# Optimization experiments

Hardware: AMD Instinct MI355X
Metric: run time of the kernel (lower is better)

Reference implementation:

```python
import jax, jax.numpy as jnp
import numpy as np

# Static configuration (from init_kwargs)
B, T, SP = 4, 100, 20          # batch, max_time_patches, max_space_patches
S = T * SP                      # flattened seq len = 2000
H, NH = 512, 8                  # hidden size, heads
D = H // NH                     # head dim = 64
CF, CB = 4, 4                   # context_forward, context_backward
ROPE_BASE = 10000.0
NEG = -1e9


def setup_inputs() -> dict:
    key = jax.random.key(0)
    ks = jax.random.split(key, 8)
    w = 1.0 / np.sqrt(H)
    x = jax.random.normal(ks[0], (B, S, H), jnp.float32)
    # token order is space-major: timestamps = time-patch id repeated per space patch
    timestamps = jnp.broadcast_to(jnp.tile(jnp.arange(T, dtype=jnp.int32), SP), (B, S))
    attn_mask = jnp.ones((B, S), jnp.int32)
    Wq = jax.random.normal(ks[1], (H, H), jnp.float32) * w
    Wk = jax.random.normal(ks[2], (H, H), jnp.float32) * w
    Wv = jax.random.normal(ks[3], (H, H), jnp.float32) * w
    Wo = jax.random.normal(ks[4], (H, H), jnp.float32) * w
    z = jnp.zeros((H,), jnp.float32)
    return {"x": x, "attn_mask": attn_mask, "timestamps": timestamps,
            "Wq": Wq, "bq": z, "Wk": Wk, "bk": z, "Wv": Wv, "bv": z,
            "Wo": Wo, "bo": z}


def _rotate_half(u):
    return jnp.concatenate((-u[..., D // 2:], u[..., :D // 2]), axis=-1)


def _rope_tables():
    inv_freq = 1.0 / (ROPE_BASE ** (jnp.arange(0, D, 2, dtype=jnp.float32) / D))
    t = jnp.arange(T, dtype=jnp.float32)
    freqs = t[:, None] * inv_freq[None, :]          # [T, D/2]
    emb = jnp.concatenate((freqs, freqs), axis=-1)  # [T, D]
    return jnp.cos(emb), jnp.sin(emb)


def _context_mask():
    # forward/backward banded window in time, tiled over space patches
    ones = jnp.ones((T, T), jnp.float32)
    m = jnp.triu(ones, k=-CF).T          # allow up to CF future time patches
    if CB > 0:
        m = m * jnp.triu(ones, k=-CB)    # allow up to CB past time patches
    return jnp.tile(m, (SP, SP))         # [S, S]


def reference(x, attn_mask, timestamps, Wq, bq, Wk, bk, Wv, bv, Wo, bo):
    # projections -> [B, NH, S, D]
    def heads(w, b):
        return (x @ w + b).reshape(B, S, NH, D).transpose(0, 2, 1, 3)
    q, k, v = heads(Wq, bq), heads(Wk, bk), heads(Wv, bv)

    # rotary position embedding indexed by time-patch timestamps
    cos_t, sin_t = _rope_tables()
    cos = cos_t[timestamps][:, None]     # [B, 1, S, D]
    sin = sin_t[timestamps][:, None]
    q = q * cos + _rotate_half(q) * sin
    k = k * cos + _rotate_half(k) * sin

    # banded-context masked attention
    scores = jnp.einsum('bhqd,bhkd->bhqk', q, k) / jnp.sqrt(jnp.float32(D))
    mask = (_context_mask()[None, None, :, :] *
            attn_mask[:, None, None, :].astype(jnp.float32)) > 0
    scores = jnp.where(mask, scores, NEG)
    attn = jax.nn.softmax(scores, axis=-1)
    out = jnp.einsum('bhqk,bhkd->bhqd', attn, v)
    out = out.transpose(0, 2, 1, 3).reshape(B, S, H)
    return out @ Wo + bo
```

## Files before the change

kernel.cpp:

```cpp
#include <hip/hip_runtime.h>
#include <hip/hip_bf16.h>
#include <stdint.h>


typedef __bf16 bf16x8 __attribute__((ext_vector_type(8)));
typedef float f32x4 __attribute__((ext_vector_type(4)));

static const size_t O_XB = 0;
static const size_t O_WT = 8192000;
static const size_t O_Q  = 10289152;
static const size_t O_K  = 18481152;
static const size_t O_V  = 26673152;
static const size_t O_RC = 34865152;
static const size_t O_RS = 34877952;
static const size_t O_VT = 34890752;

__device__ inline void gload16(const void* g, void* l) {
  __builtin_amdgcn_global_load_lds((const __attribute__((address_space(1))) void*)g,
                                   (__attribute__((address_space(3))) void*)l, 16, 0, 0);
}

__global__ __launch_bounds__(256) void prep_kernel(
    const float* __restrict__ x, const float* __restrict__ Wq, const float* __restrict__ Wk,
    const float* __restrict__ Wv, const float* __restrict__ Wo,
    __bf16* __restrict__ xb, __bf16* __restrict__ wt,
    float* __restrict__ ropeC, float* __restrict__ ropeS)
{
  const int tid = blockIdx.x * 256 + threadIdx.x;
  if (tid < 1024000) {
    float4 v = ((const float4*)x)[tid];
    union { ushort4 u; __bf16 b[4]; } p;
    p.b[0] = (__bf16)v.x; p.b[1] = (__bf16)v.y; p.b[2] = (__bf16)v.z; p.b[3] = (__bf16)v.w;
    ((ushort4*)xb)[tid] = p.u;
  }
  {
    const int mat = tid >> 18;
    const int r = tid & 262143;
    const int n = r >> 9, k = r & 511;
    const float* W = (mat == 0) ? Wq : (mat == 1) ? Wk : (mat == 2) ? Wv : Wo;
    wt[(size_t)mat * 262144 + n * 512 + k] = (__bf16)W[k * 512 + n];
  }
  if (tid < 3200) {
    const int t = tid >> 5, i = tid & 31;
    const float f = (float)t * powf(10000.0f, -(float)i / 32.0f);
    ropeC[tid] = cosf(f);
    ropeS[tid] = sinf(f);
  }
}

__device__ inline void gemm_core(const __bf16* __restrict__ A, const __bf16* __restrict__ Bm,
                                 __bf16* As, __bf16* Bs, f32x4 (&acc)[4][4],
                                 int m0, int n0, int tid, int wm, int wn, int lr, int g)
{
  const int r0 = tid >> 2;
  const int aq = tid & 3;
  for (int kk = 0; kk < 512; kk += 32) {
    int gm0 = m0 + r0;      if (gm0 > 7999) gm0 = 7999;
    int gm1 = m0 + r0 + 64; if (gm1 > 7999) gm1 = 7999;
    gload16(A + (size_t)gm0 * 512 + kk + aq * 8, As + tid * 8);
    gload16(A + (size_t)gm1 * 512 + kk + aq * 8, As + tid * 8 + 2048);
    gload16(Bm + (size_t)(n0 + r0) * 512 + kk + aq * 8, Bs + tid * 8);
    gload16(Bm + (size_t)(n0 + r0 + 64) * 512 + kk + aq * 8, Bs + tid * 8 + 2048);
    asm volatile("s_waitcnt vmcnt(0)" ::: "memory");
    __syncthreads();
    bf16x8 af[4], bfr[4];
#pragma unroll
    for (int f = 0; f < 4; ++f) {
      af[f]  = *(const bf16x8*)(As + (wm + f * 16 + lr) * 32 + g * 8);
      bfr[f] = *(const bf16x8*)(Bs + (wn + f * 16 + lr) * 32 + g * 8);
    }
#pragma unroll
    for (int i = 0; i < 4; ++i) {
#pragma unroll
      for (int j = 0; j < 4; ++j)
        acc[i][j] = __builtin_amdgcn_mfma_f32_16x16x32_bf16(af[i], bfr[j], acc[i][j], 0, 0, 0);
    }
    __syncthreads();
  }
}

__global__ __launch_bounds__(256) void qkv_gemm(
    const __bf16* __restrict__ xb, const __bf16* __restrict__ wt,
    const float* __restrict__ bq, const float* __restrict__ bk, const float* __restrict__ bv,
    const float* __restrict__ ropeC, const float* __restrict__ ropeS,
    __bf16* __restrict__ qws, __bf16* __restrict__ kws, __bf16* __restrict__ vws)
{
  const int tid = threadIdx.x;
  const int m0 = blockIdx.x * 128, n0 = blockIdx.y * 128;
  const int mat = blockIdx.z;
  __shared__ __bf16 As[4096], Bs[4096];
  f32x4 acc[4][4] = {};
  const int wid = tid >> 6, lane = tid & 63;
  const int wm = (wid >> 1) << 6, wn = (wid & 1) << 6;
  const int lr = lane & 15, g = lane >> 4;

  gemm_core(xb, wt + (size_t)mat * 262144, As, Bs, acc, m0, n0, tid, wm, wn, lr, g);

  const int hn = (n0 + wn) >> 6;
  const float* bias = (mat == 0) ? bq : (mat == 1) ? bk : bv;
  __bf16* outp = (mat == 0) ? qws : (mat == 1) ? kws : vws;
  const float qscale = (mat == 0) ? 0.125f : 1.0f;

#pragma unroll
  for (int i = 0; i < 4; ++i) {
#pragma unroll
    for (int r = 0; r < 4; ++r) {
      const int m = m0 + wm + i * 16 + g * 4 + r;
      if (m >= 8000) continue;
      const int b = m / 2000;
      const int s = m - b * 2000;
      const int t = s % 100;
      const int sp = s / 100;
      const int pos = t * 20 + sp;
      const size_t ob = ((size_t)(b * 8 + hn) * 2000 + pos) * 64;
      if (mat == 2) {
#pragma unroll
        for (int j = 0; j < 4; ++j) {
          float v = acc[i][j][r] + bias[n0 + wn + j * 16 + lr];
          outp[ob + j * 16 + lr] = (__bf16)v;
        }
      } else {
#pragma unroll
        for (int j = 0; j < 2; ++j) {
          const int dlo = j * 16 + lr;
          const float alo = acc[i][j][r]     + bias[n0 + wn + j * 16 + lr];
          const float ahi = acc[i][j + 2][r] + bias[n0 + wn + (j + 2) * 16 + lr];
          const float cs = ropeC[t * 32 + dlo], sn = ropeS[t * 32 + dlo];
          const float olo = (alo * cs - ahi * sn) * qscale;
          const float ohi = (ahi * cs + alo * sn) * qscale;
          outp[ob + dlo]      = (__bf16)olo;
          outp[ob + dlo + 32] = (__bf16)ohi;
        }
      }
    }
  }
}

__global__ __launch_bounds__(256) void vt_transpose(
    const __bf16* __restrict__ v, __bf16* __restrict__ vt)
{
  __shared__ __align__(16) __bf16 tile[64][68];
  const int tid = threadIdx.x;
  const int p0 = blockIdx.x * 64;
  const int bh = blockIdx.y;
  const __bf16* vp = v + (size_t)bh * 2000 * 64;
  __bf16* vtp = vt + (size_t)bh * 64 * 2000;
  const int np = (p0 + 64 <= 2000) ? 64 : (2000 - p0);

#pragma unroll
  for (int it = 0; it < 4; ++it) {
    const int idx = it * 256 + tid;
    const int pl = idx >> 4, d4 = (idx & 15) * 4;
    if (pl < np) {
      const ushort4 u = *(const ushort4*)(vp + (size_t)(p0 + pl) * 64 + d4);
      *(ushort4*)&tile[pl][d4] = u;
    }
  }
  __syncthreads();
#pragma unroll
  for (int it = 0; it < 16; ++it) {
    const int idx = it * 256 + tid;
    const int d = idx >> 6, p = idx & 63;
    if (p < np) vtp[(size_t)d * 2000 + p0 + p] = tile[p][d];
  }
}

__global__ __launch_bounds__(256) void attn_kernel(
    const __bf16* __restrict__ qw, const __bf16* __restrict__ kw, const __bf16* __restrict__ vt,
    const int* __restrict__ amask, __bf16* __restrict__ aout)
{
  const int wid = threadIdx.x >> 6, lane = threadIdx.x & 63;
  const int lr = lane & 15, g = lane >> 4;
  const int tq = blockIdx.x * 4 + wid;
  const int h = blockIdx.y, b = blockIdx.z;

  int t0 = tq - 4; if (t0 < 0) t0 = 0;
  int t1 = tq + 4; if (t1 > 99) t1 = 99;
  const int k0 = t0 * 20;
  const int nk = (t1 - t0 + 1) * 20;
  const int base = k0 & ~7;

  __shared__ __bf16 Pl[4][20][200];
  __shared__ float addm[4][192];

  const size_t hb = (size_t)(b * 8 + h) * 2000;
  const __bf16* qp = qw + (hb + (size_t)tq * 20) * 64;
  const __bf16* vtp = vt + (size_t)(b * 8 + h) * 64 * 2000;

  for (int k = lane; k < 192; k += 64) {
    const int kg = base + k;
    float v = -1e9f;
    if (kg >= k0 && kg < k0 + nk) {
      const int tk = kg / 20;
      const int spk = kg - tk * 20;
      if (amask[b * 2000 + spk * 100 + tk] != 0) v = 0.0f;
    }
    addm[wid][k] = v;
  }

  bf16x8 qf[2][2];
#pragma unroll
  for (int jq = 0; jq < 2; ++jq) {
    int q = jq * 16 + lr; if (q > 19) q = 19;
#pragma unroll
    for (int ks = 0; ks < 2; ++ks)
      qf[jq][ks] = *(const bf16x8*)(qp + q * 64 + ks * 32 + g * 8);
  }

  f32x4 acc[12][2] = {};
#pragma unroll
  for (int i = 0; i < 12; ++i) {
    int krow = base + i * 16 + lr; if (krow > 1999) krow = 1999;
    const __bf16* kr = kw + (hb + (size_t)krow) * 64;
    const bf16x8 af0 = *(const bf16x8*)(kr + g * 8);
    const bf16x8 af1 = *(const bf16x8*)(kr + 32 + g * 8);
    acc[i][0] = __builtin_amdgcn_mfma_f32_16x16x32_bf16(af0, qf[0][0], acc[i][0], 0, 0, 0);
    acc[i][0] = __builtin_amdgcn_mfma_f32_16x16x32_bf16(af1, qf[0][1], acc[i][0], 0, 0, 0);
    acc[i][1] = __builtin_amdgcn_mfma_f32_16x16x32_bf16(af0, qf[1][0], acc[i][1], 0, 0, 0);
    acc[i][1] = __builtin_amdgcn_mfma_f32_16x16x32_bf16(af1, qf[1][1], acc[i][1], 0, 0, 0);
  }

  __syncthreads();

#pragma unroll
  for (int jq = 0; jq < 2; ++jq) {
    float mx = -1e30f;
#pragma unroll
    for (int i = 0; i < 12; ++i)
#pragma unroll
      for (int r = 0; r < 4; ++r) {
        acc[i][jq][r] += addm[wid][i * 16 + g * 4 + r];
        mx = fmaxf(mx, acc[i][jq][r]);
      }
    mx = fmaxf(mx, __shfl_xor(mx, 16));
    mx = fmaxf(mx, __shfl_xor(mx, 32));
    float sm = 0.0f;
#pragma unroll
    for (int i = 0; i < 12; ++i)
#pragma unroll
      for (int r = 0; r < 4; ++r) {
        const float p = __expf(acc[i][jq][r] - mx);
        acc[i][jq][r] = p;
        sm += p;
      }
    sm += __shfl_xor(sm, 16);
    sm += __shfl_xor(sm, 32);
    const float rinv = 1.0f / sm;
    const int q = jq * 16 + lr;
    if (q < 20) {
#pragma unroll
      for (int i = 0; i < 12; ++i) {
        union { ushort4 u; __bf16 e[4]; } pk;
        pk.e[0] = (__bf16)(acc[i][jq][0] * rinv);
        pk.e[1] = (__bf16)(acc[i][jq][1] * rinv);
        pk.e[2] = (__bf16)(acc[i][jq][2] * rinv);
        pk.e[3] = (__bf16)(acc[i][jq][3] * rinv);
        *(ushort4*)&Pl[wid][q][i * 16 + g * 4] = pk.u;
      }
    }
  }

  __syncthreads();

  f32x4 acc2[2][4] = {};
#pragma unroll
  for (int kb = 0; kb < 6; ++kb) {
    int kv = base + kb * 32 + g * 8; if (kv >= 2000) kv = 0;
    bf16x8 bfv[4];
#pragma unroll
    for (int j2 = 0; j2 < 4; ++j2)
      bfv[j2] = *(const bf16x8*)(vtp + (size_t)(j2 * 16 + lr) * 2000 + kv);
#pragma unroll
    for (int i2 = 0; i2 < 2; ++i2) {
      int qr = i2 * 16 + lr; if (qr > 19) qr = 19;
      const bf16x8 pa = *(const bf16x8*)&Pl[wid][qr][kb * 32 + g * 8];
#pragma unroll
      for (int j2 = 0; j2 < 4; ++j2)
        acc2[i2][j2] = __builtin_amdgcn_mfma_f32_16x16x32_bf16(pa, bfv[j2], acc2[i2][j2], 0, 0, 0);
    }
  }

#pragma unroll
  for (int i2 = 0; i2 < 2; ++i2)
#pragma unroll
    for (int r = 0; r < 4; ++r) {
      const int q = i2 * 16 + g * 4 + r;
      if (q < 20) {
        const size_t ob = ((size_t)b * 2000 + q * 100 + tq) * 512 + h * 64;
#pragma unroll
        for (int j2 = 0; j2 < 4; ++j2)
          aout[ob + j2 * 16 + lr] = (__bf16)acc2[i2][j2][r];
      }
    }
}

__global__ __launch_bounds__(256) void out_gemm(
    const __bf16* __restrict__ ab, const __bf16* __restrict__ wot,
    const float* __restrict__ bo, float* __restrict__ out)
{
  const int tid = threadIdx.x;
  const int m0 = blockIdx.x * 128, n0 = blockIdx.y * 128;
  __shared__ __bf16 As[4096], Bs[4096];
  f32x4 acc[4][4] = {};
  const int wid = tid >> 6, lane = tid & 63;
  const int wm = (wid >> 1) << 6, wn = (wid & 1) << 6;
  const int lr = lane & 15, g = lane >> 4;

  gemm_core(ab, wot, As, Bs, acc, m0, n0, tid, wm, wn, lr, g);

#pragma unroll
  for (int i = 0; i < 4; ++i) {
#pragma unroll
    for (int r = 0; r < 4; ++r) {
      const int m = m0 + wm + i * 16 + g * 4 + r;
      if (m < 8000) {
#pragma unroll
        for (int j = 0; j < 4; ++j) {
          const int n = n0 + wn + j * 16 + lr;
          out[(size_t)m * 512 + n] = acc[i][j][r] + bo[n];
        }
      }
    }
  }
}

extern "C" void kernel_launch(void* const* d_in, const int* in_sizes, int n_in,
                              void* d_out, int out_size, void* d_ws, size_t ws_size,
                              hipStream_t stream) {
  const float* x   = (const float*)d_in[0];
  const int* amask = (const int*)d_in[1];
  const float* Wq = (const float*)d_in[3];
  const float* bq = (const float*)d_in[4];
  const float* Wk = (const float*)d_in[5];
  const float* bk = (const float*)d_in[6];
  const float* Wv = (const float*)d_in[7];
  const float* bv = (const float*)d_in[8];
  const float* Wo = (const float*)d_in[9];
  const float* bo = (const float*)d_in[10];
  float* out = (float*)d_out;

  char* ws = (char*)d_ws;
  __bf16* xb    = (__bf16*)(ws + O_XB);
  __bf16* wt    = (__bf16*)(ws + O_WT);
  __bf16* qws   = (__bf16*)(ws + O_Q);
  __bf16* kws   = (__bf16*)(ws + O_K);
  __bf16* vws   = (__bf16*)(ws + O_V);
  float*  ropeC = (float*)(ws + O_RC);
  float*  ropeS = (float*)(ws + O_RS);
  __bf16* vtw   = (__bf16*)(ws + O_VT);
  __bf16* aout  = (__bf16*)(ws + O_XB);

  prep_kernel<<<4096, 256, 0, stream>>>(x, Wq, Wk, Wv, Wo, xb, wt, ropeC, ropeS);
  qkv_gemm<<<dim3(63, 4, 3), 256, 0, stream>>>(xb, wt, bq, bk, bv, ropeC, ropeS, qws, kws, vws);
  vt_transpose<<<dim3(32, 32), 256, 0, stream>>>(vws, vtw);
  attn_kernel<<<dim3(25, 8, 4), 256, 0, stream>>>(qws, kws, vtw, amask, aout);
  out_gemm<<<dim3(63, 4, 1), 256, 0, stream>>>(aout, wt + 3 * 262144, bo, out);
}
```

Baseline: 91.10 us.

## Fuse x bf16 conversion into QKV GEMM, tile weight transpose, widen K-step

Removes the separate fp32-to-bf16 pass over x, so the QKV GEMM now reads fp32 x directly and converts while staging into LDS. The weight transpose in prep becomes a 64x64 shared-memory tiled transpose with coalesced reads and writes, launched on a much smaller grid. Both GEMMs move from a K step of 32 to 64, which doubles LDS tiles and halves the barrier count. The attention MFMA loops are wrapped in s_setprio raises. The trade-off is that the x loads in the QKV GEMM now pass through registers instead of direct-to-LDS loads, and each of the 4x3 column blocks re-reads and re-converts fp32 x.

```diff
diff --git a/kernel.cpp b/kernel.cpp
--- a/kernel.cpp
+++ b/kernel.cpp
@@ -6,7 +6,7 @@
 typedef __bf16 bf16x8 __attribute__((ext_vector_type(8)));
 typedef float f32x4 __attribute__((ext_vector_type(4)));
 
-static const size_t O_XB = 0;
+static const size_t O_AO = 0;
 static const size_t O_WT = 8192000;
 static const size_t O_Q  = 10289152;
 static const size_t O_K  = 18481152;
@@ -21,66 +21,95 @@
 }
 
 __global__ __launch_bounds__(256) void prep_kernel(
-    const float* __restrict__ x, const float* __restrict__ Wq, const float* __restrict__ Wk,
+    const float* __restrict__ Wq, const float* __restrict__ Wk,
     const float* __restrict__ Wv, const float* __restrict__ Wo,
-    __bf16* __restrict__ xb, __bf16* __restrict__ wt,
-    float* __restrict__ ropeC, float* __restrict__ ropeS)
-{
-  const int tid = blockIdx.x * 256 + threadIdx.x;
-  if (tid < 1024000) {
-    float4 v = ((const float4*)x)[tid];
-    union { ushort4 u; __bf16 b[4]; } p;
-    p.b[0] = (__bf16)v.x; p.b[1] = (__bf16)v.y; p.b[2] = (__bf16)v.z; p.b[3] = (__bf16)v.w;
-    ((ushort4*)xb)[tid] = p.u;
-  }
-  {
-    const int mat = tid >> 18;
-    const int r = tid & 262143;
-    const int n = r >> 9, k = r & 511;
-    const float* W = (mat == 0) ? Wq : (mat == 1) ? Wk : (mat == 2) ? Wv : Wo;
-    wt[(size_t)mat * 262144 + n * 512 + k] = (__bf16)W[k * 512 + n];
-  }
-  if (tid < 3200) {
-    const int t = tid >> 5, i = tid & 31;
-    const float f = (float)t * powf(10000.0f, -(float)i / 32.0f);
-    ropeC[tid] = cosf(f);
-    ropeS[tid] = sinf(f);
-  }
-}
-
-__device__ inline void gemm_core(const __bf16* __restrict__ A, const __bf16* __restrict__ Bm,
-                                 __bf16* As, __bf16* Bs, f32x4 (&acc)[4][4],
-                                 int m0, int n0, int tid, int wm, int wn, int lr, int g)
-{
-  const int r0 = tid >> 2;
-  const int aq = tid & 3;
-  for (int kk = 0; kk < 512; kk += 32) {
-    int gm0 = m0 + r0;      if (gm0 > 7999) gm0 = 7999;
-    int gm1 = m0 + r0 + 64; if (gm1 > 7999) gm1 = 7999;
-    gload16(A + (size_t)gm0 * 512 + kk + aq * 8, As + tid * 8);
-    gload16(A + (size_t)gm1 * 512 + kk + aq * 8, As + tid * 8 + 2048);
-    gload16(Bm + (size_t)(n0 + r0) * 512 + kk + aq * 8, Bs + tid * 8);
-    gload16(Bm + (size_t)(n0 + r0 + 64) * 512 + kk + aq * 8, Bs + tid * 8 + 2048);
+    __bf16* __restrict__ wt, float* __restrict__ ropeC, float* __restrict__ ropeS)
+{
+  __shared__ float tile[64][65];
+  const int tid = threadIdx.x;
+  const int mat = blockIdx.y;
+  const int tk = (blockIdx.x >> 3) * 64;
+  const int tn = (blockIdx.x & 7) * 64;
+  const float* W = (mat == 0) ? Wq : (mat == 1) ? Wk : (mat == 2) ? Wv : Wo;
+
+#pragma unroll
+  for (int it = 0; it < 16; ++it) {
+    const int idx = it * 256 + tid;
+    const int kl = idx >> 6, nl = idx & 63;
+    tile[kl][nl] = W[(size_t)(tk + kl) * 512 + tn + nl];
+  }
+  __syncthreads();
+#pragma unroll
+  for (int it = 0; it < 16; ++it) {
+    const int idx = it * 256 + tid;
+    const int nl = idx >> 6, kl = idx & 63;
+    wt[(size_t)mat * 262144 + (size_t)(tn + nl) * 512 + tk + kl] = (__bf16)tile[kl][nl];
+  }
+  if (blockIdx.x == 0 && mat == 0) {
+    for (int idx = tid; idx < 3200; idx += 256) {
+      const int t = idx >> 5, i = idx & 31;
+      const float f = (float)t * powf(10000.0f, -(float)i / 32.0f);
+      ropeC[idx] = cosf(f);
+      ropeS[idx] = sinf(f);
+    }
+  }
+}
+
+template<bool AF32>
+__device__ inline void gemm_core64(const void* Aptr, const __bf16* __restrict__ Bm,
+                                   __bf16* As, __bf16* Bs, f32x4 (&acc)[4][4],
+                                   int m0, int n0, int tid, int wm, int wn, int lr, int g)
+{
+  for (int kk = 0; kk < 512; kk += 64) {
+    if (AF32) {
+      const float* Af = (const float*)Aptr;
+#pragma unroll
+      for (int j = 0; j < 4; ++j) {
+        const int c = tid + j * 256;
+        int row = m0 + (c >> 3); if (row > 7999) row = 7999;
+        const float4 f0 = *(const float4*)(Af + (size_t)row * 512 + kk + (c & 7) * 8);
+        const float4 f1 = *(const float4*)(Af + (size_t)row * 512 + kk + (c & 7) * 8 + 4);
+        bf16x8 v;
+        v[0] = (__bf16)f0.x; v[1] = (__bf16)f0.y; v[2] = (__bf16)f0.z; v[3] = (__bf16)f0.w;
+        v[4] = (__bf16)f1.x; v[5] = (__bf16)f1.y; v[6] = (__bf16)f1.z; v[7] = (__bf16)f1.w;
+        *(bf16x8*)(As + c * 8) = v;
+      }
+    } else {
+      const __bf16* Ab = (const __bf16*)Aptr;
+#pragma unroll
+      for (int j = 0; j < 4; ++j) {
+        const int c = tid + j * 256;
+        int row = m0 + (c >> 3); if (row > 7999) row = 7999;
+        gload16(Ab + (size_t)row * 512 + kk + (c & 7) * 8, As + c * 8);
+      }
+    }
+#pragma unroll
+    for (int j = 0; j < 4; ++j) {
+      const int c = tid + j * 256;
+      gload16(Bm + (size_t)(n0 + (c >> 3)) * 512 + kk + (c & 7) * 8, Bs + c * 8);
+    }
     asm volatile("s_waitcnt vmcnt(0)" ::: "memory");
     __syncthreads();
-    bf16x8 af[4], bfr[4];
-#pragma unroll
-    for (int f = 0; f < 4; ++f) {
-      af[f]  = *(const bf16x8*)(As + (wm + f * 16 + lr) * 32 + g * 8);
-      bfr[f] = *(const bf16x8*)(Bs + (wn + f * 16 + lr) * 32 + g * 8);
-    }
-#pragma unroll
-    for (int i = 0; i < 4; ++i) {
-#pragma unroll
-      for (int j = 0; j < 4; ++j)
-        acc[i][j] = __builtin_amdgcn_mfma_f32_16x16x32_bf16(af[i], bfr[j], acc[i][j], 0, 0, 0);
+#pragma unroll
+    for (int ks = 0; ks < 2; ++ks) {
+      bf16x8 af[4], bfr[4];
+#pragma unroll
+      for (int f = 0; f < 4; ++f) {
+        af[f]  = *(const bf16x8*)(As + (wm + f * 16 + lr) * 64 + ks * 32 + g * 8);
+        bfr[f] = *(const bf16x8*)(Bs + (wn + f * 16 + lr) * 64 + ks * 32 + g * 8);
+      }
+#pragma unroll
+      for (int i = 0; i < 4; ++i)
+#pragma unroll
+        for (int j = 0; j < 4; ++j)
+          acc[i][j] = __builtin_amdgcn_mfma_f32_16x16x32_bf16(af[i], bfr[j], acc[i][j], 0, 0, 0);
     }
     __syncthreads();
   }
 }
 
 __global__ __launch_bounds__(256) void qkv_gemm(
-    const __bf16* __restrict__ xb, const __bf16* __restrict__ wt,
+    const float* __restrict__ x, const __bf16* __restrict__ wt,
     const float* __restrict__ bq, const float* __restrict__ bk, const float* __restrict__ bv,
     const float* __restrict__ ropeC, const float* __restrict__ ropeS,
     __bf16* __restrict__ qws, __bf16* __restrict__ kws, __bf16* __restrict__ vws)
@@ -88,13 +117,13 @@
   const int tid = threadIdx.x;
   const int m0 = blockIdx.x * 128, n0 = blockIdx.y * 128;
   const int mat = blockIdx.z;
-  __shared__ __bf16 As[4096], Bs[4096];
+  __shared__ __bf16 As[8192], Bs[8192];
   f32x4 acc[4][4] = {};
   const int wid = tid >> 6, lane = tid & 63;
   const int wm = (wid >> 1) << 6, wn = (wid & 1) << 6;
   const int lr = lane & 15, g = lane >> 4;
 
-  gemm_core(xb, wt + (size_t)mat * 262144, As, Bs, acc, m0, n0, tid, wm, wn, lr, g);
+  gemm_core64<true>(x, wt + (size_t)mat * 262144, As, Bs, acc, m0, n0, tid, wm, wn, lr, g);
 
   const int hn = (n0 + wn) >> 6;
   const float* bias = (mat == 0) ? bq : (mat == 1) ? bk : bv;
@@ -208,6 +237,7 @@
   }
 
   f32x4 acc[12][2] = {};
+  __builtin_amdgcn_s_setprio(1);
 #pragma unroll
   for (int i = 0; i < 12; ++i) {
     int krow = base + i * 16 + lr; if (krow > 1999) krow = 1999;
@@ -219,6 +249,7 @@
     acc[i][1] = __builtin_amdgcn_mfma_f32_16x16x32_bf16(af0, qf[1][0], acc[i][1], 0, 0, 0);
     acc[i][1] = __builtin_amdgcn_mfma_f32_16x16x32_bf16(af1, qf[1][1], acc[i][1], 0, 0, 0);
   }
+  __builtin_amdgcn_s_setprio(0);
 
   __syncthreads();
 
@@ -263,6 +294,7 @@
   __syncthreads();
 
   f32x4 acc2[2][4] = {};
+  __builtin_amdgcn_s_setprio(1);
 #pragma unroll
   for (int kb = 0; kb < 6; ++kb) {
     int kv = base + kb * 32 + g * 8; if (kv >= 2000) kv = 0;
@@ -279,6 +311,7 @@
         acc2[i2][j2] = __builtin_amdgcn_mfma_f32_16x16x32_bf16(pa, bfv[j2], acc2[i2][j2], 0, 0, 0);
     }
   }
+  __builtin_amdgcn_s_setprio(0);
 
 #pragma unroll
   for (int i2 = 0; i2 < 2; ++i2)
@@ -300,13 +333,13 @@
 {
   const int tid = threadIdx.x;
   const int m0 = blockIdx.x * 128, n0 = blockIdx.y * 128;
-  __shared__ __bf16 As[4096], Bs[4096];
+  __shared__ __bf16 As[8192], Bs[8192];
   f32x4 acc[4][4] = {};
   const int wid = tid >> 6, lane = tid & 63;
   const int wm = (wid >> 1) << 6, wn = (wid & 1) << 6;
   const int lr = lane & 15, g = lane >> 4;
 
-  gemm_core(ab, wot, As, Bs, acc, m0, n0, tid, wm, wn, lr, g);
+  gemm_core64<false>(ab, wot, As, Bs, acc, m0, n0, tid, wm, wn, lr, g);
 
 #pragma unroll
   for (int i = 0; i < 4; ++i) {
@@ -340,7 +373,7 @@
   float* out = (float*)d_out;
 
   char* ws = (char*)d_ws;
-  __bf16* xb    = (__bf16*)(ws + O_XB);
+  __bf16* aout  = (__bf16*)(ws + O_AO);
   __bf16* wt    = (__bf16*)(ws + O_WT);
   __bf16* qws   = (__bf16*)(ws + O_Q);
   __bf16* kws   = (__bf16*)(ws + O_K);
@@ -348,10 +381,9 @@
   float*  ropeC = (float*)(ws + O_RC);
   float*  ropeS = (float*)(ws + O_RS);
   __bf16* vtw   = (__bf16*)(ws + O_VT);
-  __bf16* aout  = (__bf16*)(ws + O_XB);
-
-  prep_kernel<<<4096, 256, 0, stream>>>(x, Wq, Wk, Wv, Wo, xb, wt, ropeC, ropeS);
-  qkv_gemm<<<dim3(63, 4, 3), 256, 0, stream>>>(xb, wt, bq, bk, bv, ropeC, ropeS, qws, kws, vws);
+
+  prep_kernel<<<dim3(64, 4), 256, 0, stream>>>(Wq, Wk, Wv, Wo, wt, ropeC, ropeS);
+  qkv_gemm<<<dim3(63, 4, 3), 256, 0, stream>>>(x, wt, bq, bk, bv, ropeC, ropeS, qws, kws, vws);
   vt_transpose<<<dim3(32, 32), 256, 0, stream>>>(vws, vtw);
   attn_kernel<<<dim3(25, 8, 4), 256, 0, stream>>>(qws, kws, vtw, amask, aout);
   out_gemm<<<dim3(63, 4, 1), 256, 0, stream>>>(aout, wt + 3 * 262144, bo, out);
```

Result: slower. 110.6 us (+21.4%).
